# Optimization experiments

Hardware: AMD Instinct MI355X
Metric: run time of the kernel (lower is better)

The kernel has to match this reference:

```python
import jax, jax.numpy as jnp
import numpy as np

B, C = 16, 256
C8 = C // 8
TH, TW = 64, 64
SH, SW = 128, 128


def setup_inputs() -> dict:
    key = jax.random.key(0)
    ks = jax.random.split(key, 9)
    scale = 1.0 / np.sqrt(C)
    # branch order: 0=t_w(alpha), 1=s_w(beta), 2=t_h(gamma), 3=s_h(omega)
    return {
        "template_map": jax.random.normal(ks[0], (B, C, TH, TW), jnp.float32),
        "scene_map": jax.random.normal(ks[1], (B, C, SH, SW), jnp.float32),
        "qw": jax.random.normal(ks[2], (4, C8, C), jnp.float32) * scale,
        "qb": jax.random.normal(ks[3], (4, C8), jnp.float32) * 0.01,
        "kw": jax.random.normal(ks[4], (4, C8, C), jnp.float32) * scale,
        "kb": jax.random.normal(ks[5], (4, C8), jnp.float32) * 0.01,
        "vw": jax.random.normal(ks[6], (4, C, C), jnp.float32) * scale,
        "vb": jax.random.normal(ks[7], (4, C), jnp.float32) * 0.01,
        # alpha, beta, gamma, omega (learned scalars; nonzero for testing)
        "scalars": jax.random.normal(ks[8], (4,), jnp.float32) * 0.1,
    }


def _proj(w, b, x):
    # 1x1 conv == per-pixel channel matmul
    return jnp.einsum("oc,bchw->bohw", w, x) + b[None, :, None, None]


def _branch(x, qw, qb, kw, kb, vw, vb, over_w):
    q = _proj(qw, qb, x)  # [B,C8,H,W]
    k = _proj(kw, kb, x)
    v = _proj(vw, vb, x)  # [B,C, H,W]
    if over_w:
        # attention over W positions; features are (C8 * H)
        e = jnp.einsum("bohw,bohv->bwv", q, k)       # [B,W,W]
        a = jax.nn.softmax(e, axis=-1)
        return jnp.einsum("bchv,bwv->bchw", v, a)     # [B,C,H,W]
    else:
        # attention over H positions; features are (C8 * W)
        e = jnp.einsum("bohw,bovw->bhv", q, k)       # [B,H,H]
        a = jax.nn.softmax(e, axis=-1)
        return jnp.einsum("bcvw,bhv->bchw", v, a)     # [B,C,H,W]


def reference(template_map, scene_map, qw, qb, kw, kb, vw, vb, scalars):
    t_out_w = scalars[0] * _branch(template_map, qw[0], qb[0], kw[0], kb[0], vw[0], vb[0], True) + template_map
    s_out_w = scalars[1] * _branch(scene_map,    qw[1], qb[1], kw[1], kb[1], vw[1], vb[1], True) + scene_map
    t_out_h = scalars[2] * _branch(template_map, qw[2], qb[2], kw[2], kb[2], vw[2], vb[2], False) + template_map
    s_out_h = scalars[3] * _branch(scene_map,    qw[3], qb[3], kw[3], kb[3], vw[3], vb[3], False) + scene_map
    return (t_out_w + t_out_h, s_out_w + s_out_h)
```

## Files before the change

kernel.cpp:

```cpp
#include <hip/hip_runtime.h>
#include <math.h>

namespace {

constexpr int Bn  = 16;
constexpr int Cn  = 256;
constexpr int C8n = 32;

typedef __attribute__((ext_vector_type(8))) __bf16 bf16x8;
typedef __attribute__((ext_vector_type(4))) __bf16 bf16x4;
typedef __attribute__((ext_vector_type(4))) float  floatx4;

__global__ __launch_bounds__(256) void qk_proj_kernel(
    const float* __restrict__ x,
    const float* __restrict__ qw,
    const float* __restrict__ qbias,
    const float* __restrict__ kw,
    const float* __restrict__ kbias,
    float* __restrict__ qo,
    float* __restrict__ ko,
    int Npix)
{
    __shared__ float xs[64][128];
    __shared__ float ws[64][68];
    const int t  = threadIdx.x;
    const int b  = blockIdx.y;
    const int p0 = blockIdx.x * 128;
    const int tx = t & 31;
    const int ty = t >> 5;
    float acc[8][4];
#pragma unroll
    for (int i = 0; i < 8; ++i)
#pragma unroll
        for (int j = 0; j < 4; ++j) acc[i][j] = 0.f;

    const float* xb  = x + (size_t)b * Cn * Npix;
    const int skk = t & 63, sor = t >> 6;

    for (int k0 = 0; k0 < Cn; k0 += 64) {
#pragma unroll
        for (int r = 0; r < 8; ++r) {
            int idx = r * 256 + t;
            int kk = idx >> 5, pp = (idx & 31) * 4;
            *(float4*)&xs[kk][pp] =
                *(const float4*)&xb[(size_t)(k0 + kk) * Npix + p0 + pp];
        }
#pragma unroll
        for (int r = 0; r < 16; ++r) {
            int o = r * 4 + sor;
            const float* wsrc = (o < 32) ? (qw + (size_t)o * Cn)
                                         : (kw + (size_t)(o - 32) * Cn);
            ws[skk][o] = wsrc[k0 + skk];
        }
        __syncthreads();
#pragma unroll 4
        for (int kk = 0; kk < 64; ++kk) {
            float4 w0 = *(const float4*)&ws[kk][ty * 8];
            float4 w1 = *(const float4*)&ws[kk][ty * 8 + 4];
            float4 xv = *(const float4*)&xs[kk][tx * 4];
            float wv[8] = {w0.x, w0.y, w0.z, w0.w, w1.x, w1.y, w1.z, w1.w};
            float pv[4] = {xv.x, xv.y, xv.z, xv.w};
#pragma unroll
            for (int i = 0; i < 8; ++i)
#pragma unroll
                for (int j = 0; j < 4; ++j)
                    acc[i][j] = fmaf(wv[i], pv[j], acc[i][j]);
        }
        __syncthreads();
    }
#pragma unroll
    for (int i = 0; i < 8; ++i) {
        int o = ty * 8 + i;
        float bias;
        float* dst;
        if (o < 32) { bias = qbias[o];      dst = qo + ((size_t)b * C8n + o)        * Npix; }
        else        { bias = kbias[o - 32]; dst = ko + ((size_t)b * C8n + (o - 32)) * Npix; }
        float4 v4 = make_float4(acc[i][0] + bias, acc[i][1] + bias,
                                acc[i][2] + bias, acc[i][3] + bias);
        *(float4*)&dst[p0 + tx * 4] = v4;
    }
}

__global__ __launch_bounds__(256) void energy_w_kernel(
    const float* __restrict__ q, const float* __restrict__ k,
    float* __restrict__ epart, int P, int KL)
{
    __shared__ float qs[32][64];
    __shared__ float ks[32][64];
    const int t  = threadIdx.x;
    const int nt = P >> 6;
    const int tw = blockIdx.x / nt;
    const int tv = blockIdx.x % nt;
    const int b  = blockIdx.y;
    const int z  = blockIdx.z;
    const int w0 = tw * 64, v0 = tv * 64;
    const int Ktot = KL * 8;
    const float* qb = q + ((size_t)b * Ktot + (size_t)z * KL) * P;
    const float* kb = k + ((size_t)b * Ktot + (size_t)z * KL) * P;
    const int tx = t & 15, ty = t >> 4;
    float acc[4][4];
#pragma unroll
    for (int i = 0; i < 4; ++i)
#pragma unroll
        for (int j = 0; j < 4; ++j) acc[i][j] = 0.f;

    for (int kc = 0; kc < KL; kc += 32) {
#pragma unroll
        for (int r = 0; r < 8; ++r) {
            int idx = r * 256 + t;
            int kk = idx >> 6, col = idx & 63;
            qs[kk][col] = qb[(size_t)(kc + kk) * P + w0 + col];
            ks[kk][col] = kb[(size_t)(kc + kk) * P + v0 + col];
        }
        __syncthreads();
#pragma unroll 8
        for (int kk = 0; kk < 32; ++kk) {
            float4 qv = *(const float4*)&qs[kk][ty * 4];
            float4 kv = *(const float4*)&ks[kk][tx * 4];
            float qa[4] = {qv.x, qv.y, qv.z, qv.w};
            float ka[4] = {kv.x, kv.y, kv.z, kv.w};
#pragma unroll
            for (int i = 0; i < 4; ++i)
#pragma unroll
                for (int j = 0; j < 4; ++j)
                    acc[i][j] = fmaf(qa[i], ka[j], acc[i][j]);
        }
        __syncthreads();
    }
#pragma unroll
    for (int i = 0; i < 4; ++i) {
        size_t off = (((size_t)z * Bn + b) * P + (w0 + ty * 4 + i)) * P + v0 + tx * 4;
        *(float4*)&epart[off] = make_float4(acc[i][0], acc[i][1], acc[i][2], acc[i][3]);
    }
}

__global__ __launch_bounds__(256) void energy_h_kernel(
    const float* __restrict__ q, const float* __restrict__ k,
    float* __restrict__ epart, int P)
{
    __shared__ float qsT[64][68];
    __shared__ float ksT[64][68];
    const int t  = threadIdx.x;
    const int nt = P >> 6;
    const int th = blockIdx.x / nt;
    const int tv = blockIdx.x % nt;
    const int b  = blockIdx.y;
    const int z  = blockIdx.z;
    const int h0 = th * 64, v0 = tv * 64;
    const int o0 = z * (C8n / 8);
    const int tx = t & 15, ty = t >> 4;
    const int ww = t & 63, hh0 = t >> 6;
    float acc[4][4];
#pragma unroll
    for (int i = 0; i < 4; ++i)
#pragma unroll
        for (int j = 0; j < 4; ++j) acc[i][j] = 0.f;

    for (int o = o0; o < o0 + 4; ++o) {
        const float* qo = q + ((size_t)(b * C8n + o)) * P * P;
        const float* ko = k + ((size_t)(b * C8n + o)) * P * P;
        for (int wc = 0; wc < P; wc += 64) {
#pragma unroll
            for (int r = 0; r < 16; ++r) {
                int hh = r * 4 + hh0;
                qsT[ww][hh] = qo[(size_t)(h0 + hh) * P + wc + ww];
                ksT[ww][hh] = ko[(size_t)(v0 + hh) * P + wc + ww];
            }
            __syncthreads();
#pragma unroll 8
            for (int kk = 0; kk < 64; ++kk) {
                float4 qv = *(const float4*)&qsT[kk][ty * 4];
                float4 kv = *(const float4*)&ksT[kk][tx * 4];
                float qa[4] = {qv.x, qv.y, qv.z, qv.w};
                float ka[4] = {kv.x, kv.y, kv.z, kv.w};
#pragma unroll
                for (int i = 0; i < 4; ++i)
#pragma unroll
                    for (int j = 0; j < 4; ++j)
                        acc[i][j] = fmaf(qa[i], ka[j], acc[i][j]);
            }
            __syncthreads();
        }
    }
#pragma unroll
    for (int i = 0; i < 4; ++i) {
        size_t off = (((size_t)z * Bn + b) * P + (h0 + ty * 4 + i)) * P + v0 + tx * 4;
        *(float4*)&epart[off] = make_float4(acc[i][0], acc[i][1], acc[i][2], acc[i][3]);
    }
}

template <int P>
__global__ __launch_bounds__(64) void softmax_kernel(
    const float* __restrict__ epart,
    __bf16* __restrict__ a)
{
    const int row  = blockIdx.x;
    const int lane = threadIdx.x;
    constexpr int E = P / 64;
    float e[E];
#pragma unroll
    for (int j = 0; j < E; ++j) {
        int v = lane + j * 64;
        float s = 0.f;
#pragma unroll
        for (int z = 0; z < 8; ++z)
            s += epart[((size_t)z * Bn * P + row) * P + v];
        e[j] = s;
    }
    float m = e[0];
#pragma unroll
    for (int j = 1; j < E; ++j) m = fmaxf(m, e[j]);
    for (int off = 32; off > 0; off >>= 1) m = fmaxf(m, __shfl_xor(m, off));
    float sum = 0.f;
#pragma unroll
    for (int j = 0; j < E; ++j) { e[j] = __expf(e[j] - m); sum += e[j]; }
    for (int off = 32; off > 0; off >>= 1) sum += __shfl_xor(sum, off);
    float inv = 1.0f / sum;
#pragma unroll
    for (int j = 0; j < E; ++j)
        a[(size_t)row * P + lane + j * 64] = (__bf16)(e[j] * inv);
}

__global__ __launch_bounds__(256) void transpose_h_kernel(
    const float* __restrict__ x, __bf16* __restrict__ xh, int P)
{
    __shared__ float tile[32][33];
    const int tpb = P >> 5;
    const int tw = blockIdx.x % tpb, th = blockIdx.x / tpb;
    const int c = blockIdx.y, b = blockIdx.z;
    const float* src = x + ((size_t)(b * Cn + c)) * P * P;
    const int i  = threadIdx.x >> 3;
    const int j4 = (threadIdx.x & 7) * 4;
    float4 v = *(const float4*)&src[(size_t)(th * 32 + i) * P + tw * 32 + j4];
    tile[i][j4 + 0] = v.x; tile[i][j4 + 1] = v.y;
    tile[i][j4 + 2] = v.z; tile[i][j4 + 3] = v.w;
    __syncthreads();
    __bf16* dst = xh + ((size_t)(b * P + tw * 32 + i) * Cn + c) * P + th * 32 + j4;
    bf16x4 o = { (__bf16)tile[j4 + 0][i], (__bf16)tile[j4 + 1][i],
                 (__bf16)tile[j4 + 2][i], (__bf16)tile[j4 + 3][i] };
    *(bf16x4*)dst = o;
}

__global__ __launch_bounds__(256) void cvt_vw_kernel(
    const float* __restrict__ vw, __bf16* __restrict__ vwb)
{
    int i4 = blockIdx.x * 256 + threadIdx.x;
    float4 v = *(const float4*)&vw[(size_t)i4 * 4];
    bf16x4 o = { (__bf16)v.x, (__bf16)v.y, (__bf16)v.z, (__bf16)v.w };
    *(bf16x4*)&vwb[(size_t)i4 * 4] = o;
}

template <int P, int BM, int BN, int MODE>
__global__ __launch_bounds__(256) void mix_mfma_kernel(
    const __bf16* __restrict__ abf,
    const float*  __restrict__ x,
    const __bf16* __restrict__ xh,
    __bf16* __restrict__ yt)
{
    constexpr int BK  = 32;
    constexpr int LDA = BK + 8;
    constexpr int WNn = BN / 64;
    __shared__ __bf16 As[BM][LDA];
    __shared__ __bf16 Bs[BN][LDA];
    __shared__ __bf16 Es[4][16][72];
    const int t = threadIdx.x;
    const int z = blockIdx.y;
    const int b = z / P, j = z % P;
    const int mt = blockIdx.x / (Cn / BN);
    const int nt = blockIdx.x % (Cn / BN);
    const int m0 = mt * BM, n0 = nt * BN;
    const int wave = t >> 6, lane = t & 63;
    const int wm = (wave / WNn) * 64, wn = (wave % WNn) * 64;
    const int l16 = lane & 15, quad = lane >> 4;

    floatx4 acc[4][4] = {};

    const __bf16* Ab = abf + (size_t)b * P * P + (size_t)m0 * P;

    for (int kc = 0; kc < P; kc += BK) {
#pragma unroll
        for (int r = 0; r < BM * 4 / 256; ++r) {
            int ch = r * 256 + t;
            int row = ch >> 2, part = ch & 3;
            *(uint4*)&As[row][part * 8] =
                *(const uint4*)&Ab[(size_t)row * P + kc + part * 8];
        }
#pragma unroll
        for (int r = 0; r < BN * 4 / 256; ++r) {
            int ch = r * 256 + t;
            int row = ch >> 2, part = ch & 3;
            if (MODE == 0) {
                const float* src =
                    x + ((size_t)(b * Cn + n0 + row) * P + j) * P + kc + part * 8;
                float4 v0 = *(const float4*)&src[0];
                float4 v1 = *(const float4*)&src[4];
                bf16x8 o = { (__bf16)v0.x, (__bf16)v0.y, (__bf16)v0.z, (__bf16)v0.w,
                             (__bf16)v1.x, (__bf16)v1.y, (__bf16)v1.z, (__bf16)v1.w };
                *(bf16x8*)&Bs[row][part * 8] = o;
            } else {
                *(uint4*)&Bs[row][part * 8] =
                    *(const uint4*)&xh[((size_t)(b * P + j) * Cn + n0 + row) * P + kc + part * 8];
            }
        }
        __syncthreads();
        bf16x8 af[4], bfr[4];
#pragma unroll
        for (int i = 0; i < 4; ++i)
            af[i] = *(const bf16x8*)&As[wm + i * 16 + l16][quad * 8];
#pragma unroll
        for (int j2 = 0; j2 < 4; ++j2)
            bfr[j2] = *(const bf16x8*)&Bs[wn + j2 * 16 + l16][quad * 8];
#pragma unroll
        for (int i = 0; i < 4; ++i)
#pragma unroll
            for (int j2 = 0; j2 < 4; ++j2)
                acc[i][j2] = __builtin_amdgcn_mfma_f32_16x16x32_bf16(
                    af[i], bfr[j2], acc[i][j2], 0, 0, 0);
        __syncthreads();
    }

    const size_t outB = (size_t)b * P * P * Cn;
#pragma unroll
    for (int i = 0; i < 4; ++i) {
#pragma unroll
        for (int j2 = 0; j2 < 4; ++j2)
#pragma unroll
            for (int r = 0; r < 4; ++r)
                Es[wave][quad * 4 + r][j2 * 16 + l16] = (__bf16)acc[i][j2][r];
#pragma unroll
        for (int s = 0; s < 2; ++s) {
            int ch = s * 64 + lane;
            int row = ch >> 3, part = ch & 7;
            bf16x8 v = *(const bf16x8*)&Es[wave][row][part * 8];
            int m = m0 + wm + i * 16 + row;
            size_t rowOff = (MODE == 0) ? (size_t)(j * P + m) : ((size_t)m * P + j);
            *(bf16x8*)&yt[outB + rowOff * Cn + n0 + wn + part * 8] = v;
        }
    }
}

__global__ __launch_bounds__(256) void vproj_mfma_kernel(
    const __bf16* __restrict__ yt,
    const __bf16* __restrict__ vwb,
    const float* __restrict__ vb,
    const float* __restrict__ x,
    float* __restrict__ out,
    const float* __restrict__ scal, int si, int first, int Npix)
{
    constexpr int BK = 32, LDA = 40;
    __shared__ __bf16 As[128][LDA];
    __shared__ __bf16 Bs[128][LDA];
    const int t  = threadIdx.x;
    const int p0 = blockIdx.x * 128;
    const int c0 = blockIdx.y * 128;
    const int b  = blockIdx.z;
    const int wave = t >> 6, lane = t & 63;
    const int wm = (wave >> 1) * 64, wn = (wave & 1) * 64;
    const int l16 = lane & 15, quad = lane >> 4;
    floatx4 acc[4][4] = {};
    const __bf16* Ab = vwb + (size_t)c0 * Cn;
    const __bf16* Bb = yt + ((size_t)b * Npix + p0) * Cn;

    for (int kc = 0; kc < Cn; kc += BK) {
#pragma unroll
        for (int r = 0; r < 2; ++r) {
            int ch = r * 256 + t;
            int row = ch >> 2, part = ch & 3;
            *(uint4*)&As[row][part * 8] =
                *(const uint4*)&Ab[(size_t)row * Cn + kc + part * 8];
            *(uint4*)&Bs[row][part * 8] =
                *(const uint4*)&Bb[(size_t)row * Cn + kc + part * 8];
        }
        __syncthreads();
        bf16x8 af[4], bfr[4];
#pragma unroll
        for (int i = 0; i < 4; ++i)
            af[i] = *(const bf16x8*)&As[wm + i * 16 + l16][quad * 8];
#pragma unroll
        for (int j2 = 0; j2 < 4; ++j2)
            bfr[j2] = *(const bf16x8*)&Bs[wn + j2 * 16 + l16][quad * 8];
#pragma unroll
        for (int i = 0; i < 4; ++i)
#pragma unroll
            for (int j2 = 0; j2 < 4; ++j2)
                acc[i][j2] = __builtin_amdgcn_mfma_f32_16x16x32_bf16(
                    af[i], bfr[j2], acc[i][j2], 0, 0, 0);
        __syncthreads();
    }

    const float s = scal[si];
#pragma unroll
    for (int i = 0; i < 4; ++i)
#pragma unroll
        for (int r = 0; r < 4; ++r) {
            int c = c0 + wm + i * 16 + quad * 4 + r;
            float bias = vb[c];
            size_t base = ((size_t)(b * Cn + c)) * Npix + p0 + wn + l16;
#pragma unroll
            for (int j2 = 0; j2 < 4; ++j2) {
                size_t idx = base + (size_t)j2 * 16;
                float vres = s * (acc[i][j2][r] + bias);
                vres += first ? 2.f * x[idx] : out[idx];
                out[idx] = vres;
            }
        }
}

struct Bufs {
    __bf16* XH;
    __bf16* YT;
    float*  E;
    __bf16* ABF;
    __bf16* VWB;
    float*  Q;
    float*  K;
};

void run_image(const float* x, float* out, int P, int brW, int brH,
               const float* qw, const float* qb, const float* kw, const float* kb,
               const float* vb, const float* sc,
               const Bufs& w, hipStream_t stream)
{
    const int Npix = P * P;
    dim3 blk(256);
    dim3 eg((P / 64) * (P / 64), Bn, 8);

    qk_proj_kernel<<<dim3(Npix / 128, Bn), blk, 0, stream>>>(
        x, qw + (size_t)brW * C8n * Cn, qb + (size_t)brW * C8n,
        kw + (size_t)brW * C8n * Cn, kb + (size_t)brW * C8n, w.Q, w.K, Npix);
    energy_w_kernel<<<eg, blk, 0, stream>>>(w.Q, w.K, w.E, P, C8n * P / 8);
    if (P == 64) {
        softmax_kernel<64><<<Bn * P, 64, 0, stream>>>(w.E, w.ABF);
        mix_mfma_kernel<64, 64, 256, 0><<<dim3(1, Bn * 64), blk, 0, stream>>>(
            w.ABF, x, w.XH, w.YT);
    } else {
        softmax_kernel<128><<<Bn * P, 64, 0, stream>>>(w.E, w.ABF);
        mix_mfma_kernel<128, 128, 128, 0><<<dim3(2, Bn * 128), blk, 0, stream>>>(
            w.ABF, x, w.XH, w.YT);
    }
    vproj_mfma_kernel<<<dim3(Npix / 128, 2, Bn), blk, 0, stream>>>(
        w.YT, w.VWB + (size_t)brW * Cn * Cn, vb + (size_t)brW * Cn,
        x, out, sc, brW, 1, Npix);

    transpose_h_kernel<<<dim3((P / 32) * (P / 32), Cn, Bn), blk, 0, stream>>>(
        x, w.XH, P);
    qk_proj_kernel<<<dim3(Npix / 128, Bn), blk, 0, stream>>>(
        x, qw + (size_t)brH * C8n * Cn, qb + (size_t)brH * C8n,
        kw + (size_t)brH * C8n * Cn, kb + (size_t)brH * C8n, w.Q, w.K, Npix);
    energy_h_kernel<<<eg, blk, 0, stream>>>(w.Q, w.K, w.E, P);
    if (P == 64) {
        softmax_kernel<64><<<Bn * P, 64, 0, stream>>>(w.E, w.ABF);
        mix_mfma_kernel<64, 64, 256, 1><<<dim3(1, Bn * 64), blk, 0, stream>>>(
            w.ABF, x, w.XH, w.YT);
    } else {
        softmax_kernel<128><<<Bn * P, 64, 0, stream>>>(w.E, w.ABF);
        mix_mfma_kernel<128, 128, 128, 1><<<dim3(2, Bn * 128), blk, 0, stream>>>(
            w.ABF, x, w.XH, w.YT);
    }
    vproj_mfma_kernel<<<dim3(Npix / 128, 2, Bn), blk, 0, stream>>>(
        w.YT, w.VWB + (size_t)brH * Cn * Cn, vb + (size_t)brH * Cn,
        x, out, sc, brH, 0, Npix);
}

}

extern "C" void kernel_launch(void* const* d_in, const int* in_sizes, int n_in,
                              void* d_out, int out_size, void* d_ws, size_t ws_size,
                              hipStream_t stream) {
    (void)in_sizes; (void)n_in; (void)out_size; (void)ws_size;
    const float* tmap = (const float*)d_in[0];
    const float* smap = (const float*)d_in[1];
    const float* qw   = (const float*)d_in[2];
    const float* qb   = (const float*)d_in[3];
    const float* kw   = (const float*)d_in[4];
    const float* kb   = (const float*)d_in[5];
    const float* vw   = (const float*)d_in[6];
    const float* vb   = (const float*)d_in[7];
    const float* sc   = (const float*)d_in[8];

    float* out0 = (float*)d_out;
    float* out1 = out0 + (size_t)16 * 256 * 64 * 64;

    char* p = (char*)d_ws;
    Bufs w;
    w.XH  = (__bf16*)p;                 p += (size_t)134217728;
    w.YT  = (__bf16*)p;                 p += (size_t)134217728;
    w.E   = (float*)p;                  p += (size_t)8388608;
    w.ABF = (__bf16*)p;                 p += (size_t)524288;
    w.VWB = (__bf16*)p;                 p += (size_t)524288;
    w.Q   = (float*)w.YT;
    w.K   = (float*)w.YT + (size_t)16 * 32 * 16384;

    cvt_vw_kernel<<<dim3(256), 256, 0, stream>>>(vw, w.VWB);

    run_image(tmap, out0, 64, 0, 2, qw, qb, kw, kb, vb, sc, w, stream);
    run_image(smap, out1, 128, 1, 3, qw, qb, kw, kb, vb, sc, w, stream);
}
```

Before: 1.691 ms.

## Double-buffer LDS tiles with register prefetch and vectorize vproj epilogue via LDS

Both MFMA GEMM kernels (mix and vproj) now stage the next K tile in registers while computing on the current LDS buffer. Alternating between two LDS buffers removes one barrier per iteration. The vproj epilogue is restaged through LDS so the residual read-modify-write uses float4 row-contiguous accesses instead of scattered scalar ones, and a launch-bounds occupancy hint of 3 blocks per CU is added. The cost is more LDS and register use, which may lower occupancy.

Result: faster. 1.601 ms (-5.3%).

```diff
diff --git a/kernel.cpp b/kernel.cpp
--- a/kernel.cpp
+++ b/kernel.cpp
@@ -260,8 +260,11 @@
     constexpr int BK  = 32;
     constexpr int LDA = BK + 8;
     constexpr int WNn = BN / 64;
-    __shared__ __bf16 As[BM][LDA];
-    __shared__ __bf16 Bs[BN][LDA];
+    constexpr int ACH = BM / 64;
+    constexpr int BCH = BN / 64;
+    constexpr int NT  = P / BK;
+    __shared__ __bf16 As[2][BM][LDA];
+    __shared__ __bf16 Bs[2][BN][LDA];
     __shared__ __bf16 Es[4][16][72];
     const int t = threadIdx.x;
     const int z = blockIdx.y;
@@ -272,51 +275,73 @@
     const int wave = t >> 6, lane = t & 63;
     const int wm = (wave / WNn) * 64, wn = (wave % WNn) * 64;
     const int l16 = lane & 15, quad = lane >> 4;
+    const int crow = t >> 2, cpart = (t & 3) * 8;
 
     floatx4 acc[4][4] = {};
 
     const __bf16* Ab = abf + (size_t)b * P * P + (size_t)m0 * P;
 
-    for (int kc = 0; kc < P; kc += BK) {
-#pragma unroll
-        for (int r = 0; r < BM * 4 / 256; ++r) {
-            int ch = r * 256 + t;
-            int row = ch >> 2, part = ch & 3;
-            *(uint4*)&As[row][part * 8] =
-                *(const uint4*)&Ab[(size_t)row * P + kc + part * 8];
-        }
-#pragma unroll
-        for (int r = 0; r < BN * 4 / 256; ++r) {
-            int ch = r * 256 + t;
-            int row = ch >> 2, part = ch & 3;
+    uint4  aR[ACH];
+    float4 bRa[BCH], bRb[BCH];
+    uint4  bRu[BCH];
+
+    auto load_tile = [&](int kc) {
+#pragma unroll
+        for (int r = 0; r < ACH; ++r) {
+            int row = r * 64 + crow;
+            aR[r] = *(const uint4*)&Ab[(size_t)row * P + kc + cpart];
+        }
+#pragma unroll
+        for (int r = 0; r < BCH; ++r) {
+            int row = r * 64 + crow;
             if (MODE == 0) {
                 const float* src =
-                    x + ((size_t)(b * Cn + n0 + row) * P + j) * P + kc + part * 8;
-                float4 v0 = *(const float4*)&src[0];
-                float4 v1 = *(const float4*)&src[4];
-                bf16x8 o = { (__bf16)v0.x, (__bf16)v0.y, (__bf16)v0.z, (__bf16)v0.w,
-                             (__bf16)v1.x, (__bf16)v1.y, (__bf16)v1.z, (__bf16)v1.w };
-                *(bf16x8*)&Bs[row][part * 8] = o;
+                    x + ((size_t)(b * Cn + n0 + row) * P + j) * P + kc + cpart;
+                bRa[r] = *(const float4*)&src[0];
+                bRb[r] = *(const float4*)&src[4];
             } else {
-                *(uint4*)&Bs[row][part * 8] =
-                    *(const uint4*)&xh[((size_t)(b * P + j) * Cn + n0 + row) * P + kc + part * 8];
+                bRu[r] = *(const uint4*)&xh[((size_t)(b * P + j) * Cn + n0 + row) * P + kc + cpart];
             }
         }
+    };
+    auto store_tile = [&](int buf) {
+#pragma unroll
+        for (int r = 0; r < ACH; ++r)
+            *(uint4*)&As[buf][r * 64 + crow][cpart] = aR[r];
+#pragma unroll
+        for (int r = 0; r < BCH; ++r) {
+            if (MODE == 0) {
+                bf16x8 o = { (__bf16)bRa[r].x, (__bf16)bRa[r].y,
+                             (__bf16)bRa[r].z, (__bf16)bRa[r].w,
+                             (__bf16)bRb[r].x, (__bf16)bRb[r].y,
+                             (__bf16)bRb[r].z, (__bf16)bRb[r].w };
+                *(bf16x8*)&Bs[buf][r * 64 + crow][cpart] = o;
+            } else {
+                *(uint4*)&Bs[buf][r * 64 + crow][cpart] = bRu[r];
+            }
+        }
+    };
+
+    load_tile(0);
+#pragma unroll
+    for (int it = 0; it < NT; ++it) {
+        const int buf = it & 1;
+        store_tile(buf);
         __syncthreads();
+        if (it < NT - 1) load_tile((it + 1) * BK);
         bf16x8 af[4], bfr[4];
 #pragma unroll
         for (int i = 0; i < 4; ++i)
-            af[i] = *(const bf16x8*)&As[wm + i * 16 + l16][quad * 8];
+            af[i] = *(const bf16x8*)&As[buf][wm + i * 16 + l16][quad * 8];
 #pragma unroll
         for (int j2 = 0; j2 < 4; ++j2)
-            bfr[j2] = *(const bf16x8*)&Bs[wn + j2 * 16 + l16][quad * 8];
+            bfr[j2] = *(const bf16x8*)&Bs[buf][wn + j2 * 16 + l16][quad * 8];
 #pragma unroll
         for (int i = 0; i < 4; ++i)
 #pragma unroll
             for (int j2 = 0; j2 < 4; ++j2)
                 acc[i][j2] = __builtin_amdgcn_mfma_f32_16x16x32_bf16(
                     af[i], bfr[j2], acc[i][j2], 0, 0, 0);
-        __syncthreads();
     }
 
     const size_t outB = (size_t)b * P * P * Cn;
@@ -328,8 +353,8 @@
             for (int r = 0; r < 4; ++r)
                 Es[wave][quad * 4 + r][j2 * 16 + l16] = (__bf16)acc[i][j2][r];
 #pragma unroll
-        for (int s = 0; s < 2; ++s) {
-            int ch = s * 64 + lane;
+        for (int s2 = 0; s2 < 2; ++s2) {
+            int ch = s2 * 64 + lane;
             int row = ch >> 3, part = ch & 7;
             bf16x8 v = *(const bf16x8*)&Es[wave][row][part * 8];
             int m = m0 + wm + i * 16 + row;
@@ -339,7 +364,7 @@
     }
 }
 
-__global__ __launch_bounds__(256) void vproj_mfma_kernel(
+__global__ __launch_bounds__(256, 3) void vproj_mfma_kernel(
     const __bf16* __restrict__ yt,
     const __bf16* __restrict__ vwb,
     const float* __restrict__ vb,
@@ -347,9 +372,10 @@
     float* __restrict__ out,
     const float* __restrict__ scal, int si, int first, int Npix)
 {
-    constexpr int BK = 32, LDA = 40;
-    __shared__ __bf16 As[128][LDA];
-    __shared__ __bf16 Bs[128][LDA];
+    __shared__ __align__(16) char smraw[40960];
+    __bf16 (*As)[128][40]  = (__bf16(*)[128][40])(smraw);
+    __bf16 (*Bsm)[128][40] = (__bf16(*)[128][40])(smraw + 20480);
+
     const int t  = threadIdx.x;
     const int p0 = blockIdx.x * 128;
     const int c0 = blockIdx.y * 128;
@@ -357,53 +383,76 @@
     const int wave = t >> 6, lane = t & 63;
     const int wm = (wave >> 1) * 64, wn = (wave & 1) * 64;
     const int l16 = lane & 15, quad = lane >> 4;
+    const int crow = t >> 2, cpart = (t & 3) * 8;
     floatx4 acc[4][4] = {};
     const __bf16* Ab = vwb + (size_t)c0 * Cn;
     const __bf16* Bb = yt + ((size_t)b * Npix + p0) * Cn;
 
-    for (int kc = 0; kc < Cn; kc += BK) {
-#pragma unroll
-        for (int r = 0; r < 2; ++r) {
-            int ch = r * 256 + t;
-            int row = ch >> 2, part = ch & 3;
-            *(uint4*)&As[row][part * 8] =
-                *(const uint4*)&Ab[(size_t)row * Cn + kc + part * 8];
-            *(uint4*)&Bs[row][part * 8] =
-                *(const uint4*)&Bb[(size_t)row * Cn + kc + part * 8];
-        }
+    uint4 aR0, aR1, bR0, bR1;
+    auto load_tile = [&](int kc) {
+        aR0 = *(const uint4*)&Ab[(size_t)crow * Cn + kc + cpart];
+        aR1 = *(const uint4*)&Ab[(size_t)(crow + 64) * Cn + kc + cpart];
+        bR0 = *(const uint4*)&Bb[(size_t)crow * Cn + kc + cpart];
+        bR1 = *(const uint4*)&Bb[(size_t)(crow + 64) * Cn + kc + cpart];
+    };
+
+    load_tile(0);
+#pragma unroll
+    for (int it = 0; it < 8; ++it) {
+        const int buf = it & 1;
+        *(uint4*)&As[buf][crow][cpart]       = aR0;
+        *(uint4*)&As[buf][crow + 64][cpart]  = aR1;
+        *(uint4*)&Bsm[buf][crow][cpart]      = bR0;
+        *(uint4*)&Bsm[buf][crow + 64][cpart] = bR1;
         __syncthreads();
+        if (it < 7) load_tile((it + 1) * 32);
         bf16x8 af[4], bfr[4];
 #pragma unroll
         for (int i = 0; i < 4; ++i)
-            af[i] = *(const bf16x8*)&As[wm + i * 16 + l16][quad * 8];
+            af[i] = *(const bf16x8*)&As[buf][wm + i * 16 + l16][quad * 8];
 #pragma unroll
         for (int j2 = 0; j2 < 4; ++j2)
-            bfr[j2] = *(const bf16x8*)&Bs[wn + j2 * 16 + l16][quad * 8];
+            bfr[j2] = *(const bf16x8*)&Bsm[buf][wn + j2 * 16 + l16][quad * 8];
 #pragma unroll
         for (int i = 0; i < 4; ++i)
 #pragma unroll
             for (int j2 = 0; j2 < 4; ++j2)
                 acc[i][j2] = __builtin_amdgcn_mfma_f32_16x16x32_bf16(
                     af[i], bfr[j2], acc[i][j2], 0, 0, 0);
-        __syncthreads();
-    }
+    }
+    __syncthreads();
 
     const float s = scal[si];
-#pragma unroll
-    for (int i = 0; i < 4; ++i)
-#pragma unroll
-        for (int r = 0; r < 4; ++r) {
-            int c = c0 + wm + i * 16 + quad * 4 + r;
+    float* ewp = (float*)smraw + wave * (16 * 68);
+#pragma unroll
+    for (int i = 0; i < 4; ++i) {
+#pragma unroll
+        for (int j2 = 0; j2 < 4; ++j2)
+#pragma unroll
+            for (int r = 0; r < 4; ++r)
+                ewp[(quad * 4 + r) * 68 + j2 * 16 + l16] = acc[i][j2][r];
+#pragma unroll
+        for (int u = 0; u < 4; ++u) {
+            int idx = u * 64 + lane;
+            int rr = idx >> 4, col = (idx & 15) * 4;
+            float4 v = *(const float4*)&ewp[rr * 68 + col];
+            int c = c0 + wm + i * 16 + rr;
             float bias = vb[c];
-            size_t base = ((size_t)(b * Cn + c)) * Npix + p0 + wn + l16;
-#pragma unroll
-            for (int j2 = 0; j2 < 4; ++j2) {
-                size_t idx = base + (size_t)j2 * 16;
-                float vres = s * (acc[i][j2][r] + bias);
-                vres += first ? 2.f * x[idx] : out[idx];
-                out[idx] = vres;
+            size_t g = ((size_t)(b * Cn + c)) * Npix + p0 + wn + col;
+            float4 prev;
+            if (first) {
+                float4 xv = *(const float4*)&x[g];
+                prev = make_float4(2.f * xv.x, 2.f * xv.y, 2.f * xv.z, 2.f * xv.w);
+            } else {
+                prev = *(const float4*)&out[g];
             }
-        }
+            float4 res = make_float4(s * (v.x + bias) + prev.x,
+                                     s * (v.y + bias) + prev.y,
+                                     s * (v.z + bias) + prev.z,
+                                     s * (v.w + bias) + prev.w);
+            *(float4*)&out[g] = res;
+        }
+    }
 }
 
 struct Bufs {
```
